# Performance work log

Measured on AMD Instinct MI355X. Metric: run time of the kernel, lower is better.

The kernel has to match this reference:

```python
import jax, jax.numpy as jnp
import numpy as np

N_HEADS = 16
EPS = 1e-6

def _split_heads(x, h):
    b, t, d = x.shape
    return x.reshape(b, t, h, d // h).transpose(0, 2, 1, 3)  # b h t e

def _elu_fm(x):
    # elu(x) + 1, the default feature map
    return jax.nn.elu(x) + 1.0

def setup_inputs() -> dict:
    key = jax.random.key(0)
    kq, kk, kv = jax.random.split(key, 3)
    shape = (4, 4096, 1024)
    return {
        "query": jax.random.normal(kq, shape, dtype=jnp.float32),
        "key": jax.random.normal(kk, shape, dtype=jnp.float32),
        "value": jax.random.normal(kv, shape, dtype=jnp.float32),
    }

def reference(query, key, value):
    q = _split_heads(query, N_HEADS)   # b h t e
    k = _split_heads(key, N_HEADS)     # b h s e
    v = _split_heads(value, N_HEADS)   # b h s d
    Q = _elu_fm(q)
    K = _elu_fm(k)
    # non-causal linear attention (attn_mask=None path)
    k_sum = K.sum(axis=-2)                                   # b h e
    D_inv = 1.0 / (jnp.einsum('bhne,bhe->bhn', Q, k_sum) + EPS)
    context = jnp.einsum('bhse,bhsd->bhed', K, v)            # b h e d
    out = jnp.einsum('bhed,bhne,bhn->bhnd', context, Q, D_inv)
    b, h, t, d = out.shape
    return out.transpose(0, 2, 1, 3).reshape(b, t, h * d)    # b t (h d)
```

## Files before the change

kernel.cpp:

```cpp
#include <hip/hip_runtime.h>
#include <cmath>

#define T_SEQ 4096
#define D_MODEL 1024
#define EPS 1e-6f
#define CHUNKS 16
#define RSTRIDE 257

typedef __attribute__((ext_vector_type(8))) short bf16x8;
typedef __attribute__((ext_vector_type(4))) float f32x4;

__device__ __forceinline__ float elu1(float x) { return x > 0.f ? x + 1.f : __expf(x); }

__device__ __forceinline__ unsigned f2bf_u(float f) {
    union { float f; unsigned u; } v; v.f = f;
    unsigned r = v.u + 0x7fffu + ((v.u >> 16) & 1u);
    return r >> 16;
}
__device__ __forceinline__ short f2bf(float f) { return (short)f2bf_u(f); }
__device__ __forceinline__ unsigned cvt_pk_bf16(float lo, float hi) {
    unsigned r;
    asm("v_cvt_pk_bf16_f32 %0, %1, %2" : "=v"(r) : "v"(lo), "v"(hi));
    return r;
}

__global__ __launch_bounds__(1024) void ctx_fused(const float* __restrict__ K,
                                                  const float* __restrict__ V,
                                                  float* __restrict__ partial) {
    __shared__ __align__(16) float sL[2][2][32 * RSTRIDE];

    const int bb = blockIdx.x >> 6;
    const int hq = (blockIdx.x >> 4) & 3;
    const int ch = blockIdx.x & 15;
    const int tid = threadIdx.x;
    const int wave = tid >> 6, lane = tid & 63;
    const int hh = wave >> 2, qd = wave & 3, eh = qd >> 1, dh = qd & 1;
    const int g = lane >> 4, r = lane & 15;
    const int u = wave;

    const size_t base = (size_t)bb * T_SEQ * D_MODEL;
    const int s0 = ch * 256;
    const int colb = hq * 256;

    f32x4 acc[2][2], accs[2];
#pragma unroll
    for (int i = 0; i < 2; ++i)
#pragma unroll
        for (int q = 0; q < 4; ++q) { accs[i][q] = 0.f; acc[i][0][q] = 0.f; acc[i][1][q] = 0.f; }

    bf16x8 ones;
    const short ob = (r == 0) ? (short)0x3F80 : (short)0;
#pragma unroll
    for (int j = 0; j < 8; ++j) ones[j] = ob;

    union U8 { unsigned u[4]; bf16x8 v; };

    auto stage = [&](int t, int buf) {
        const size_t gr = base + (size_t)(s0 + 32 * t + 2 * u) * D_MODEL + colb + 4 * lane;
        const float* Kp = K + gr;
        const float* Vp = V + gr;
        float* dK = &sL[buf][0][(2 * u) * RSTRIDE];
        float* dV = &sL[buf][1][(2 * u) * RSTRIDE];
        __builtin_amdgcn_global_load_lds((const unsigned*)Kp, (unsigned*)dK, 16, 0, 0);
        __builtin_amdgcn_global_load_lds((const unsigned*)(Kp + D_MODEL),
                                         (unsigned*)(dK + RSTRIDE), 16, 0, 0);
        __builtin_amdgcn_global_load_lds((const unsigned*)Vp, (unsigned*)dV, 16, 0, 0);
        __builtin_amdgcn_global_load_lds((const unsigned*)(Vp + D_MODEL),
                                         (unsigned*)(dV + RSTRIDE), 16, 0, 0);
    };

    auto compute = [&](int buf) {
        const float* tk = &sL[buf][0][0];
        const float* tv = &sL[buf][1][0];
        const int hb = hh * 64;
        bf16x8 a[2], bv[2];
#pragma unroll
        for (int mi = 0; mi < 2; ++mi) {
            const int col = hb + 32 * eh + 16 * mi + r;
            float f[8];
#pragma unroll
            for (int j = 0; j < 8; ++j) f[j] = tk[(8 * g + j) * RSTRIDE + col];
            U8 t;
            t.u[0] = cvt_pk_bf16(elu1(f[0]), elu1(f[1]));
            t.u[1] = cvt_pk_bf16(elu1(f[2]), elu1(f[3]));
            t.u[2] = cvt_pk_bf16(elu1(f[4]), elu1(f[5]));
            t.u[3] = cvt_pk_bf16(elu1(f[6]), elu1(f[7]));
            a[mi] = t.v;
        }
#pragma unroll
        for (int ni = 0; ni < 2; ++ni) {
            const int col = hb + 32 * dh + 16 * ni + r;
            float f[8];
#pragma unroll
            for (int j = 0; j < 8; ++j) f[j] = tv[(8 * g + j) * RSTRIDE + col];
            U8 t;
            t.u[0] = cvt_pk_bf16(f[0], f[1]);
            t.u[1] = cvt_pk_bf16(f[2], f[3]);
            t.u[2] = cvt_pk_bf16(f[4], f[5]);
            t.u[3] = cvt_pk_bf16(f[6], f[7]);
            bv[ni] = t.v;
        }
#pragma unroll
        for (int mi = 0; mi < 2; ++mi) {
#pragma unroll
            for (int ni = 0; ni < 2; ++ni)
                acc[mi][ni] = __builtin_amdgcn_mfma_f32_16x16x32_bf16(a[mi], bv[ni], acc[mi][ni], 0, 0, 0);
            if (dh == 0)
                accs[mi] = __builtin_amdgcn_mfma_f32_16x16x32_bf16(a[mi], ones, accs[mi], 0, 0, 0);
        }
    };

    stage(0, 0);
    __syncthreads();
#pragma unroll 1
    for (int t = 0; t < 8; ++t) {
        if (t < 7) stage(t + 1, (t + 1) & 1);
        compute(t & 1);
        __syncthreads();
    }

    float* slab = partial + ((size_t)((bb * 16 + hq * 4 + hh) * CHUNKS + ch)) * 4160;
#pragma unroll
    for (int mi = 0; mi < 2; ++mi)
#pragma unroll
        for (int ni = 0; ni < 2; ++ni)
            *(f32x4*)&slab[qd * 1024 + (mi * 2 + ni) * 256 + lane * 4] = acc[mi][ni];
    if (dh == 0 && r == 0) {
#pragma unroll
        for (int mi = 0; mi < 2; ++mi)
#pragma unroll
            for (int q = 0; q < 4; ++q)
                slab[4096 + 32 * eh + 16 * mi + 4 * g + q] = accs[mi][q];
    }
}

__global__ __launch_bounds__(256) void ctx_reduce(const float* __restrict__ partial,
                                                  ushort* __restrict__ ctxbf) {
    const int head = blockIdx.x >> 2, part = blockIdx.x & 3;
    const float* pbase = partial + (size_t)head * CHUNKS * 4160;
    ushort* cbase = ctxbf + (size_t)head * 4160;
    const int lo = part * 260;
    for (int i4 = lo + threadIdx.x; i4 < lo + 260; i4 += 256) {
        f32x4 s;
#pragma unroll
        for (int k = 0; k < 4; ++k) s[k] = 0.f;
#pragma unroll
        for (int c = 0; c < CHUNKS; ++c) {
            const f32x4 v = *(const f32x4*)&pbase[(size_t)c * 4160 + i4 * 4];
#pragma unroll
            for (int k = 0; k < 4; ++k) s[k] += v[k];
        }
        const int f0 = i4 * 4;
        if (f0 < 4096) {
#pragma unroll
            for (int k = 0; k < 4; ++k) {
                const int f = f0 + k;
                const int qd = f >> 10, t2 = (f >> 8) & 3, ln = (f >> 2) & 63, q = f & 3;
                const int e = 32 * (qd >> 1) + 16 * (t2 >> 1) + 4 * (ln >> 4) + q;
                const int d = 32 * (qd & 1) + 16 * (t2 & 1) + (ln & 15);
                cbase[d * 64 + e] = (ushort)f2bf(s[k]);
            }
        } else {
#pragma unroll
            for (int k = 0; k < 4; ++k) cbase[f0 + k] = (ushort)f2bf(s[k]);
        }
    }
}

__global__ __launch_bounds__(256, 4) void attn_out(const float* __restrict__ Q,
                                                   const ushort* __restrict__ ctxbf,
                                                   float* __restrict__ out) {
    const int head = blockIdx.x >> 4, nb = blockIdx.x & 15;
    const int b = head >> 4, h = head & 15;
    const int tid = threadIdx.x, wave = tid >> 6, lane = tid & 63;
    const int g = lane >> 4, r = lane & 15;
    const ushort* C = ctxbf + (size_t)head * 4160;

    bf16x8 bfr[2][5];
#pragma unroll
    for (int kt = 0; kt < 2; ++kt) {
#pragma unroll
        for (int n = 0; n < 4; ++n)
            bfr[kt][n] = *(const bf16x8*)&C[(16 * n + r) * 64 + kt * 32 + 8 * g];
        bf16x8 ks = *(const bf16x8*)&C[4096 + kt * 32 + 8 * g];
        if (r != 0) {
#pragma unroll
            for (int j = 0; j < 8; ++j) ks[j] = 0;
        }
        bfr[kt][4] = ks;
    }

    const int n0 = nb * 256 + wave * 64;
    const float* qbase = Q + ((size_t)b * T_SEQ + n0) * D_MODEL + (size_t)h * 64;

    f32x4 acc[4][5];
#pragma unroll
    for (int m = 0; m < 4; ++m)
#pragma unroll
        for (int n = 0; n < 5; ++n)
#pragma unroll
            for (int q = 0; q < 4; ++q) acc[m][n][q] = 0.f;

    union U8 { unsigned u[4]; bf16x8 v; };
#pragma unroll
    for (int kt = 0; kt < 2; ++kt)
#pragma unroll
        for (int m = 0; m < 4; ++m) {
            const float* qp = qbase + (size_t)(16 * m + r) * D_MODEL + kt * 32 + 8 * g;
            const float4 q1 = *(const float4*)qp;
            const float4 q2 = *(const float4*)(qp + 4);
            U8 a;
            a.u[0] = cvt_pk_bf16(elu1(q1.x), elu1(q1.y));
            a.u[1] = cvt_pk_bf16(elu1(q1.z), elu1(q1.w));
            a.u[2] = cvt_pk_bf16(elu1(q2.x), elu1(q2.y));
            a.u[3] = cvt_pk_bf16(elu1(q2.z), elu1(q2.w));
#pragma unroll
            for (int n = 0; n < 5; ++n)
                acc[m][n] = __builtin_amdgcn_mfma_f32_16x16x32_bf16(a.v, bfr[kt][n], acc[m][n], 0, 0, 0);
        }

#pragma unroll
    for (int m = 0; m < 4; ++m) {
        float dinv[4];
#pragma unroll
        for (int q = 0; q < 4; ++q)
            dinv[q] = 1.f / (__shfl(acc[m][4][q], lane & 48) + EPS);
#pragma unroll
        for (int q = 0; q < 4; ++q) {
            float* op = out + ((size_t)b * T_SEQ + n0 + 16 * m + 4 * g + q) * D_MODEL
                        + (size_t)h * 64 + r;
#pragma unroll
            for (int n = 0; n < 4; ++n) op[16 * n] = acc[m][n][q] * dinv[q];
        }
    }
}

extern "C" void kernel_launch(void* const* d_in, const int* in_sizes, int n_in,
                              void* d_out, int out_size, void* d_ws, size_t ws_size,
                              hipStream_t stream) {
    const float* Q = (const float*)d_in[0];
    const float* K = (const float*)d_in[1];
    const float* V = (const float*)d_in[2];
    float* out = (float*)d_out;

    float* partial  = out;
    ushort* ctxbf   = (ushort*)d_ws;

    hipLaunchKernelGGL(ctx_fused,  dim3(256),  dim3(1024), 0, stream, K, V, partial);
    hipLaunchKernelGGL(ctx_reduce, dim3(256),  dim3(256),  0, stream, partial, ctxbf);
    hipLaunchKernelGGL(attn_out,   dim3(1024), dim3(256),  0, stream, Q, ctxbf, out);
}
```

Before: 57.90 us.

## Store bf16 partials and stage Q tiles through LDS with async loads

The per-chunk context partials are now written and reduced as bf16 instead of fp32, which halves the partial-slab traffic. The output kernel is rebuilt as a 1024-thread block covering four heads over 256 rows. It double-buffers contiguous 256-column Q tiles into LDS with global_load_lds, replacing per-lane strided float4 global loads. The bf16 partials lose precision before the sum across 16 chunks. The new kernel also has fewer blocks (256) and uses large LDS, which limits occupancy.

```diff
diff --git a/kernel.cpp b/kernel.cpp
--- a/kernel.cpp
+++ b/kernel.cpp
@@ -23,10 +23,14 @@
     asm("v_cvt_pk_bf16_f32 %0, %1, %2" : "=v"(r) : "v"(lo), "v"(hi));
     return r;
 }
+__device__ __forceinline__ float bf2f(unsigned short s) {
+    union { unsigned u; float f; } v; v.u = ((unsigned)s) << 16;
+    return v.f;
+}
 
 __global__ __launch_bounds__(1024) void ctx_fused(const float* __restrict__ K,
                                                   const float* __restrict__ V,
-                                                  float* __restrict__ partial) {
+                                                  unsigned short* __restrict__ partial) {
     __shared__ __align__(16) float sL[2][2][32 * RSTRIDE];
 
     const int bb = blockIdx.x >> 6;
@@ -119,36 +123,40 @@
         __syncthreads();
     }
 
-    float* slab = partial + ((size_t)((bb * 16 + hq * 4 + hh) * CHUNKS + ch)) * 4160;
+    unsigned short* slab = partial + ((size_t)((bb * 16 + hq * 4 + hh) * CHUNKS + ch)) * 4160;
 #pragma unroll
     for (int mi = 0; mi < 2; ++mi)
 #pragma unroll
-        for (int ni = 0; ni < 2; ++ni)
-            *(f32x4*)&slab[qd * 1024 + (mi * 2 + ni) * 256 + lane * 4] = acc[mi][ni];
+        for (int ni = 0; ni < 2; ++ni) {
+            uint2 w;
+            w.x = cvt_pk_bf16(acc[mi][ni][0], acc[mi][ni][1]);
+            w.y = cvt_pk_bf16(acc[mi][ni][2], acc[mi][ni][3]);
+            *(uint2*)&slab[qd * 1024 + (mi * 2 + ni) * 256 + lane * 4] = w;
+        }
     if (dh == 0 && r == 0) {
 #pragma unroll
-        for (int mi = 0; mi < 2; ++mi)
-#pragma unroll
-            for (int q = 0; q < 4; ++q)
-                slab[4096 + 32 * eh + 16 * mi + 4 * g + q] = accs[mi][q];
-    }
-}
-
-__global__ __launch_bounds__(256) void ctx_reduce(const float* __restrict__ partial,
-                                                  ushort* __restrict__ ctxbf) {
+        for (int mi = 0; mi < 2; ++mi) {
+            uint2 w;
+            w.x = cvt_pk_bf16(accs[mi][0], accs[mi][1]);
+            w.y = cvt_pk_bf16(accs[mi][2], accs[mi][3]);
+            *(uint2*)&slab[4096 + 32 * eh + 16 * mi + 4 * g] = w;
+        }
+    }
+}
+
+__global__ __launch_bounds__(256) void ctx_reduce(const unsigned short* __restrict__ partial,
+                                                  unsigned short* __restrict__ ctxbf) {
     const int head = blockIdx.x >> 2, part = blockIdx.x & 3;
-    const float* pbase = partial + (size_t)head * CHUNKS * 4160;
-    ushort* cbase = ctxbf + (size_t)head * 4160;
+    const unsigned short* pbase = partial + (size_t)head * CHUNKS * 4160;
+    unsigned short* cbase = ctxbf + (size_t)head * 4160;
     const int lo = part * 260;
     for (int i4 = lo + threadIdx.x; i4 < lo + 260; i4 += 256) {
-        f32x4 s;
-#pragma unroll
-        for (int k = 0; k < 4; ++k) s[k] = 0.f;
+        float s[4] = {0.f, 0.f, 0.f, 0.f};
 #pragma unroll
         for (int c = 0; c < CHUNKS; ++c) {
-            const f32x4 v = *(const f32x4*)&pbase[(size_t)c * 4160 + i4 * 4];
-#pragma unroll
-            for (int k = 0; k < 4; ++k) s[k] += v[k];
+            const ushort4 v = *(const ushort4*)&pbase[(size_t)c * 4160 + i4 * 4];
+            s[0] += bf2f(v.x); s[1] += bf2f(v.y);
+            s[2] += bf2f(v.z); s[3] += bf2f(v.w);
         }
         const int f0 = i4 * 4;
         if (f0 < 4096) {
@@ -158,24 +166,35 @@
                 const int qd = f >> 10, t2 = (f >> 8) & 3, ln = (f >> 2) & 63, q = f & 3;
                 const int e = 32 * (qd >> 1) + 16 * (t2 >> 1) + 4 * (ln >> 4) + q;
                 const int d = 32 * (qd & 1) + 16 * (t2 & 1) + (ln & 15);
-                cbase[d * 64 + e] = (ushort)f2bf(s[k]);
+                cbase[d * 64 + e] = (unsigned short)f2bf(s[k]);
             }
         } else {
 #pragma unroll
-            for (int k = 0; k < 4; ++k) cbase[f0 + k] = (ushort)f2bf(s[k]);
-        }
-    }
-}
-
-__global__ __launch_bounds__(256, 4) void attn_out(const float* __restrict__ Q,
-                                                   const ushort* __restrict__ ctxbf,
+            for (int k = 0; k < 4; ++k) cbase[f0 + k] = (unsigned short)f2bf(s[k]);
+        }
+    }
+}
+
+__global__ __launch_bounds__(1024) void attn_fused(const float* __restrict__ Q,
+                                                   const unsigned short* __restrict__ ctxbf,
                                                    float* __restrict__ out) {
-    const int head = blockIdx.x >> 4, nb = blockIdx.x & 15;
-    const int b = head >> 4, h = head & 15;
-    const int tid = threadIdx.x, wave = tid >> 6, lane = tid & 63;
+    __shared__ __align__(16) float sQ[2][64 * RSTRIDE];
+
+    const int bb = blockIdx.x >> 6;
+    const int hq = (blockIdx.x >> 4) & 3;
+    const int ch = blockIdx.x & 15;
+    const int tid = threadIdx.x;
+    const int wave = tid >> 6, lane = tid & 63;
+    const int hh = wave >> 2, mp = wave & 3;
     const int g = lane >> 4, r = lane & 15;
-    const ushort* C = ctxbf + (size_t)head * 4160;
-
+    const int u = wave;
+
+    const int head = bb * 16 + hq * 4 + hh;
+    const size_t qb = (size_t)bb * T_SEQ * D_MODEL;
+    const int n0 = ch * 256;
+    const int colb = hq * 256;
+
+    const unsigned short* C = ctxbf + (size_t)head * 4160;
     bf16x8 bfr[2][5];
 #pragma unroll
     for (int kt = 0; kt < 2; ++kt) {
@@ -190,48 +209,62 @@
         bfr[kt][4] = ks;
     }
 
-    const int n0 = nb * 256 + wave * 64;
-    const float* qbase = Q + ((size_t)b * T_SEQ + n0) * D_MODEL + (size_t)h * 64;
-
-    f32x4 acc[4][5];
-#pragma unroll
-    for (int m = 0; m < 4; ++m)
+    union U8 { unsigned u[4]; bf16x8 v; };
+
+    auto stage = [&](int tl, int buf) {
+        const float* Qp = Q + qb + (size_t)(n0 + 64 * tl + 4 * u) * D_MODEL + colb + 4 * lane;
+        float* dst = &sQ[buf][(4 * u) * RSTRIDE];
+#pragma unroll
+        for (int i = 0; i < 4; ++i)
+            __builtin_amdgcn_global_load_lds((const unsigned*)(Qp + (size_t)i * D_MODEL),
+                                             (unsigned*)(dst + i * RSTRIDE), 16, 0, 0);
+    };
+
+    auto compute = [&](int tl, int buf) {
+        const float* tq = &sQ[buf][0];
+        f32x4 acc[5];
 #pragma unroll
         for (int n = 0; n < 5; ++n)
 #pragma unroll
-            for (int q = 0; q < 4; ++q) acc[m][n][q] = 0.f;
-
-    union U8 { unsigned u[4]; bf16x8 v; };
-#pragma unroll
-    for (int kt = 0; kt < 2; ++kt)
-#pragma unroll
-        for (int m = 0; m < 4; ++m) {
-            const float* qp = qbase + (size_t)(16 * m + r) * D_MODEL + kt * 32 + 8 * g;
-            const float4 q1 = *(const float4*)qp;
-            const float4 q2 = *(const float4*)(qp + 4);
+            for (int q = 0; q < 4; ++q) acc[n][q] = 0.f;
+
+#pragma unroll
+        for (int kt = 0; kt < 2; ++kt) {
+            const float* p = &tq[(16 * mp + r) * RSTRIDE + hh * 64 + kt * 32 + 8 * g];
+            float f[8];
+#pragma unroll
+            for (int j = 0; j < 8; ++j) f[j] = p[j];
             U8 a;
-            a.u[0] = cvt_pk_bf16(elu1(q1.x), elu1(q1.y));
-            a.u[1] = cvt_pk_bf16(elu1(q1.z), elu1(q1.w));
-            a.u[2] = cvt_pk_bf16(elu1(q2.x), elu1(q2.y));
-            a.u[3] = cvt_pk_bf16(elu1(q2.z), elu1(q2.w));
+            a.u[0] = cvt_pk_bf16(elu1(f[0]), elu1(f[1]));
+            a.u[1] = cvt_pk_bf16(elu1(f[2]), elu1(f[3]));
+            a.u[2] = cvt_pk_bf16(elu1(f[4]), elu1(f[5]));
+            a.u[3] = cvt_pk_bf16(elu1(f[6]), elu1(f[7]));
 #pragma unroll
             for (int n = 0; n < 5; ++n)
-                acc[m][n] = __builtin_amdgcn_mfma_f32_16x16x32_bf16(a.v, bfr[kt][n], acc[m][n], 0, 0, 0);
-        }
-
-#pragma unroll
-    for (int m = 0; m < 4; ++m) {
+                acc[n] = __builtin_amdgcn_mfma_f32_16x16x32_bf16(a.v, bfr[kt][n], acc[n], 0, 0, 0);
+        }
+
         float dinv[4];
 #pragma unroll
         for (int q = 0; q < 4; ++q)
-            dinv[q] = 1.f / (__shfl(acc[m][4][q], lane & 48) + EPS);
+            dinv[q] = 1.f / (__shfl(acc[4][q], lane & 48) + EPS);
+        const int rowb = n0 + 64 * tl + 16 * mp;
 #pragma unroll
         for (int q = 0; q < 4; ++q) {
-            float* op = out + ((size_t)b * T_SEQ + n0 + 16 * m + 4 * g + q) * D_MODEL
-                        + (size_t)h * 64 + r;
-#pragma unroll
-            for (int n = 0; n < 4; ++n) op[16 * n] = acc[m][n][q] * dinv[q];
-        }
+            float* op = out + ((size_t)bb * T_SEQ + rowb + 4 * g + q) * D_MODEL
+                        + (size_t)(hq * 4 + hh) * 64 + r;
+#pragma unroll
+            for (int n = 0; n < 4; ++n) op[16 * n] = acc[n][q] * dinv[q];
+        }
+    };
+
+    stage(0, 0);
+    __syncthreads();
+#pragma unroll 1
+    for (int tl = 0; tl < 4; ++tl) {
+        if (tl < 3) stage(tl + 1, (tl + 1) & 1);
+        compute(tl, tl & 1);
+        __syncthreads();
     }
 }
 
@@ -243,10 +276,10 @@
     const float* V = (const float*)d_in[2];
     float* out = (float*)d_out;
 
-    float* partial  = out;
-    ushort* ctxbf   = (ushort*)d_ws;
-
-    hipLaunchKernelGGL(ctx_fused,  dim3(256),  dim3(1024), 0, stream, K, V, partial);
-    hipLaunchKernelGGL(ctx_reduce, dim3(256),  dim3(256),  0, stream, partial, ctxbf);
-    hipLaunchKernelGGL(attn_out,   dim3(1024), dim3(256),  0, stream, Q, ctxbf, out);
-}
+    unsigned short* partial = (unsigned short*)d_out;
+    unsigned short* ctxbf   = (unsigned short*)d_ws;
+
+    hipLaunchKernelGGL(ctx_fused,  dim3(256), dim3(1024), 0, stream, K, V, partial);
+    hipLaunchKernelGGL(ctx_reduce, dim3(256), dim3(256),  0, stream, partial, ctxbf);
+    hipLaunchKernelGGL(attn_fused, dim3(256), dim3(1024), 0, stream, Q, ctxbf, out);
+}
```

Result: slower. 61.10 us (+5.5%).

## Store context partials in bf16 and relax barriers with explicit vmcnt waits

Applied to the files above, without the earlier changes.

The per-chunk partial context sums are now packed to bf16 before being written to the scratch area, and the reduce kernel reads bf16 and accumulates in fp32. This halves the partial-sum write and read traffic. The main loop's __syncthreads calls are replaced by raw s_barrier plus partial vmcnt waits and sched_barriers, so the next stage's global loads can stay in flight during compute. The cost is extra rounding on partials before the sum, and correctness now depends on the hand-set vmcnt count matching the number of outstanding loads per stage.

```diff
diff --git a/kernel.cpp b/kernel.cpp
--- a/kernel.cpp
+++ b/kernel.cpp
@@ -23,10 +23,14 @@
     asm("v_cvt_pk_bf16_f32 %0, %1, %2" : "=v"(r) : "v"(lo), "v"(hi));
     return r;
 }
+__device__ __forceinline__ float bf2f(unsigned short s) {
+    union { unsigned u; float f; } v; v.u = ((unsigned)s) << 16;
+    return v.f;
+}
 
 __global__ __launch_bounds__(1024) void ctx_fused(const float* __restrict__ K,
                                                   const float* __restrict__ V,
-                                                  float* __restrict__ partial) {
+                                                  unsigned short* __restrict__ partial) {
     __shared__ __align__(16) float sL[2][2][32 * RSTRIDE];
 
     const int bb = blockIdx.x >> 6;
@@ -111,44 +115,56 @@
     };
 
     stage(0, 0);
-    __syncthreads();
 #pragma unroll 1
     for (int t = 0; t < 8; ++t) {
-        if (t < 7) stage(t + 1, (t + 1) & 1);
+        if (t < 7) {
+            stage(t + 1, (t + 1) & 1);
+            asm volatile("s_waitcnt vmcnt(4)" ::: "memory");
+        } else {
+            asm volatile("s_waitcnt vmcnt(0)" ::: "memory");
+        }
+        __builtin_amdgcn_s_barrier();
+        __builtin_amdgcn_sched_barrier(0);
         compute(t & 1);
-        __syncthreads();
-    }
-
-    float* slab = partial + ((size_t)((bb * 16 + hq * 4 + hh) * CHUNKS + ch)) * 4160;
+        __builtin_amdgcn_sched_barrier(0);
+        asm volatile("" ::: "memory");
+        __builtin_amdgcn_s_barrier();
+    }
+
+    unsigned short* slab = partial + ((size_t)((bb * 16 + hq * 4 + hh) * CHUNKS + ch)) * 4160;
 #pragma unroll
     for (int mi = 0; mi < 2; ++mi)
 #pragma unroll
-        for (int ni = 0; ni < 2; ++ni)
-            *(f32x4*)&slab[qd * 1024 + (mi * 2 + ni) * 256 + lane * 4] = acc[mi][ni];
+        for (int ni = 0; ni < 2; ++ni) {
+            uint2 w;
+            w.x = cvt_pk_bf16(acc[mi][ni][0], acc[mi][ni][1]);
+            w.y = cvt_pk_bf16(acc[mi][ni][2], acc[mi][ni][3]);
+            *(uint2*)&slab[qd * 1024 + (mi * 2 + ni) * 256 + lane * 4] = w;
+        }
     if (dh == 0 && r == 0) {
 #pragma unroll
-        for (int mi = 0; mi < 2; ++mi)
-#pragma unroll
-            for (int q = 0; q < 4; ++q)
-                slab[4096 + 32 * eh + 16 * mi + 4 * g + q] = accs[mi][q];
-    }
-}
-
-__global__ __launch_bounds__(256) void ctx_reduce(const float* __restrict__ partial,
-                                                  ushort* __restrict__ ctxbf) {
+        for (int mi = 0; mi < 2; ++mi) {
+            uint2 w;
+            w.x = cvt_pk_bf16(accs[mi][0], accs[mi][1]);
+            w.y = cvt_pk_bf16(accs[mi][2], accs[mi][3]);
+            *(uint2*)&slab[4096 + 32 * eh + 16 * mi + 4 * g] = w;
+        }
+    }
+}
+
+__global__ __launch_bounds__(256) void ctx_reduce(const unsigned short* __restrict__ partial,
+                                                  unsigned short* __restrict__ ctxbf) {
     const int head = blockIdx.x >> 2, part = blockIdx.x & 3;
-    const float* pbase = partial + (size_t)head * CHUNKS * 4160;
-    ushort* cbase = ctxbf + (size_t)head * 4160;
+    const unsigned short* pbase = partial + (size_t)head * CHUNKS * 4160;
+    unsigned short* cbase = ctxbf + (size_t)head * 4160;
     const int lo = part * 260;
     for (int i4 = lo + threadIdx.x; i4 < lo + 260; i4 += 256) {
-        f32x4 s;
-#pragma unroll
-        for (int k = 0; k < 4; ++k) s[k] = 0.f;
+        float s[4] = {0.f, 0.f, 0.f, 0.f};
 #pragma unroll
         for (int c = 0; c < CHUNKS; ++c) {
-            const f32x4 v = *(const f32x4*)&pbase[(size_t)c * 4160 + i4 * 4];
-#pragma unroll
-            for (int k = 0; k < 4; ++k) s[k] += v[k];
+            const ushort4 v = *(const ushort4*)&pbase[(size_t)c * 4160 + i4 * 4];
+            s[0] += bf2f(v.x); s[1] += bf2f(v.y);
+            s[2] += bf2f(v.z); s[3] += bf2f(v.w);
         }
         const int f0 = i4 * 4;
         if (f0 < 4096) {
@@ -158,23 +174,23 @@
                 const int qd = f >> 10, t2 = (f >> 8) & 3, ln = (f >> 2) & 63, q = f & 3;
                 const int e = 32 * (qd >> 1) + 16 * (t2 >> 1) + 4 * (ln >> 4) + q;
                 const int d = 32 * (qd & 1) + 16 * (t2 & 1) + (ln & 15);
-                cbase[d * 64 + e] = (ushort)f2bf(s[k]);
+                cbase[d * 64 + e] = (unsigned short)f2bf(s[k]);
             }
         } else {
 #pragma unroll
-            for (int k = 0; k < 4; ++k) cbase[f0 + k] = (ushort)f2bf(s[k]);
+            for (int k = 0; k < 4; ++k) cbase[f0 + k] = (unsigned short)f2bf(s[k]);
         }
     }
 }
 
 __global__ __launch_bounds__(256, 4) void attn_out(const float* __restrict__ Q,
-                                                   const ushort* __restrict__ ctxbf,
+                                                   const unsigned short* __restrict__ ctxbf,
                                                    float* __restrict__ out) {
     const int head = blockIdx.x >> 4, nb = blockIdx.x & 15;
     const int b = head >> 4, h = head & 15;
     const int tid = threadIdx.x, wave = tid >> 6, lane = tid & 63;
     const int g = lane >> 4, r = lane & 15;
-    const ushort* C = ctxbf + (size_t)head * 4160;
+    const unsigned short* C = ctxbf + (size_t)head * 4160;
 
     bf16x8 bfr[2][5];
 #pragma unroll
@@ -243,8 +259,8 @@
     const float* V = (const float*)d_in[2];
     float* out = (float*)d_out;
 
-    float* partial  = out;
-    ushort* ctxbf   = (ushort*)d_ws;
+    unsigned short* partial = (unsigned short*)d_out;
+    unsigned short* ctxbf   = (unsigned short*)d_ws;
 
     hipLaunchKernelGGL(ctx_fused,  dim3(256),  dim3(1024), 0, stream, K, V, partial);
     hipLaunchKernelGGL(ctx_reduce, dim3(256),  dim3(256),  0, stream, partial, ctxbf);
```

Measured after the change: 56.74 us, median of 3. 2.0% less time.
